# Optimization experiments

Measured on AMD Instinct MI355X. Metric: run time of the kernel, lower is better.

The kernel has to match this reference:

```python
import jax, jax.numpy as jnp
import numpy as np

B, C, H, W = 32, 512, 256, 14
NSEL = 7  # 7 even columns (0,2,..,12) on even rows, 7 odd columns (1,3,..,13) on odd rows


def setup_inputs() -> dict:
    key = jax.random.key(0)
    kx, kp = jax.random.split(key)
    x = jax.random.normal(kx, (B, C, H, W), dtype=jnp.float32)
    # per-(batch,row) random permutation of the 7 selected columns
    pkeys = jax.random.split(kp, B * H)
    perms = jax.vmap(lambda k: jax.random.permutation(k, NSEL))(pkeys)
    perms = perms.reshape(B, H, NSEL).astype(jnp.int32)
    return {"x": x, "perms": perms}


def reference(x, perms):
    # Even rows shuffle columns {0,2,...,12}; odd rows shuffle {1,3,...,13}.
    # Column of the j-th selected element on row h: 2*j + (h % 2).
    parity = (jnp.arange(H) % 2).astype(jnp.int32)[None, :, None]      # [1,H,1]
    dst = 2 * jnp.arange(NSEL, dtype=jnp.int32)[None, None, :] + parity  # [1,H,7] -> broadcast [B,H,7]
    dst = jnp.broadcast_to(dst, (B, H, NSEL))
    src = 2 * perms + parity                                            # [B,H,7]
    # Build a per-(b,h) column remap: identity, with dst <- src on shuffled slots.
    colmap = jnp.broadcast_to(jnp.arange(W, dtype=jnp.int32), (B, H, W))
    bi = jnp.arange(B, dtype=jnp.int32)[:, None, None]
    hi = jnp.arange(H, dtype=jnp.int32)[None, :, None]
    colmap = colmap.at[bi, hi, dst].set(src)                            # [B,H,W]
    # Single vectorized gather along the width axis, broadcast over channels.
    idx = jnp.broadcast_to(colmap[:, None, :, :], (B, C, H, W))
    return jnp.take_along_axis(x, idx, axis=3)
```

## Files before the change

kernel.cpp:

```cpp
#include <hip/hip_runtime.h>


#define TILE_ROWS   512
#define TILE_FLOATS (TILE_ROWS * 14)
#define TILE_V4     (TILE_FLOATS / 4)
#define WAVE_V4     448

typedef float v4f __attribute__((ext_vector_type(4)));

#define GLOAD_LDS16(gp, lp)                                                   \
    __builtin_amdgcn_global_load_lds(                                         \
        (const __attribute__((address_space(1))) void*)(gp),                  \
        (__attribute__((address_space(3))) void*)(lp), 16, 0, 0)

__global__ __launch_bounds__(256, 5) void GSRS_shuffle_pipe7_kernel(
    const float* __restrict__ x,
    const int* __restrict__ perms,
    float* __restrict__ out)
{
    __shared__ float tile[TILE_FLOATS];
    __shared__ unsigned char cmap[256][16];

    const unsigned tid  = threadIdx.x;
    const unsigned lane = tid & 63u;
    const unsigned wv   = tid >> 6;
    const unsigned tb   = blockIdx.x;
    const unsigned base = tb * TILE_FLOATS;
    const unsigned b    = tb >> 8;
    const unsigned q0   = wv * WAVE_V4 + lane;

    const unsigned r0 = wv * 128u + 2u * lane;
    const unsigned h0 = r0 & 255u;
    const int* pr = perms + b * 1792u + h0 * 7u;
    int pm[14];
#pragma unroll
    for (int j = 0; j < 7; ++j) {
        int2 t2 = *reinterpret_cast<const int2*>(pr + 2 * j);
        pm[2 * j] = t2.x; pm[2 * j + 1] = t2.y;
    }
    __builtin_amdgcn_sched_barrier(0);

    const v4f* xv = reinterpret_cast<const v4f*>(x + base);
    v4f*       tv = reinterpret_cast<v4f*>(tile);
#pragma unroll
    for (int i = 0; i < 7; ++i)
        GLOAD_LDS16(xv + q0 + i * 64, tv + q0 + i * 64);
    __builtin_amdgcn_sched_barrier(0);

    {
#pragma unroll
        for (int rr = 0; rr < 2; ++rr) {
            const unsigned h = h0 + rr;
            const unsigned p = h & 1u;
            union { unsigned char c[16]; uint4 v; } u;
#pragma unroll
            for (int w14 = 0; w14 < 14; ++w14) {
                unsigned src = (((unsigned)w14 & 1u) == p)
                    ? 2u * (unsigned)pm[rr * 7 + (w14 >> 1)] + p
                    : (unsigned)w14;
                u.c[w14] = (unsigned char)src;
            }
            u.c[14] = 0; u.c[15] = 0;
            *reinterpret_cast<uint4*>(&cmap[h][0]) = u.v;
        }
    }

    v4f vbuf[7];
#pragma unroll
    for (int i = 0; i < 7; ++i) {
        if (i < 6) {
            asm volatile("s_waitcnt vmcnt(%0)" :: "i"(5 - i) : "memory");
            __builtin_amdgcn_sched_barrier(0);
        }
        const unsigned q  = q0 + i * 64;
        unsigned lo   = q * 4u;
        unsigned lrow = lo / 14u;
        unsigned w14  = lo - lrow * 14u;
        v4f v;
#pragma unroll
        for (int k4 = 0; k4 < 4; ++k4) {
            const unsigned h   = lrow & 255u;
            const unsigned src = cmap[h][w14];
            v[k4] = tile[lrow * 14u + src];
            if (++w14 == 14u) { w14 = 0u; ++lrow; }
        }
        vbuf[i] = v;
    }

    v4f* ov = reinterpret_cast<v4f*>(out + base);
#pragma unroll
    for (int i = 0; i < 7; ++i)
        __builtin_nontemporal_store(vbuf[i], ov + q0 + i * 64);
}

extern "C" void kernel_launch(void* const* d_in, const int* in_sizes, int n_in,
                              void* d_out, int out_size, void* d_ws, size_t ws_size,
                              hipStream_t stream) {
    const float* x     = (const float*)d_in[0];
    const int*   perms = (const int*)d_in[1];
    float*       out   = (float*)d_out;

    hipLaunchKernelGGL(GSRS_shuffle_pipe7_kernel, dim3(8192), dim3(256), 0, stream,
                       x, perms, out);
}
```

Measured before the change: 72.36 us.

## Halve tile size, use per-thread row cmap and scalar coalesced stores

Shrinks each block's tile to 256 rows and doubles the grid, raising the occupancy bound to 8 blocks. Each thread builds the column map for one row, loads are issued by 56 lanes per wave in four chunks, and output is written as scalar nontemporal floats, one per lane per step. The aim is more blocks in flight and simpler index math, at the cost of narrower stores and more store instructions.

Result: no change. 72.06 us (-0.4%).

```diff
diff --git a/kernel.cpp b/kernel.cpp
--- a/kernel.cpp
+++ b/kernel.cpp
@@ -1,10 +1,10 @@
 #include <hip/hip_runtime.h>
 
 
-#define TILE_ROWS   512
+#define TILE_ROWS   256
 #define TILE_FLOATS (TILE_ROWS * 14)
-#define TILE_V4     (TILE_FLOATS / 4)
-#define WAVE_V4     448
+#define WAVE_F      896
+#define WAVE_V4     224
 
 typedef float v4f __attribute__((ext_vector_type(4)));
 
@@ -13,7 +13,7 @@
         (const __attribute__((address_space(1))) void*)(gp),                  \
         (__attribute__((address_space(3))) void*)(lp), 16, 0, 0)
 
-__global__ __launch_bounds__(256, 5) void GSRS_shuffle_pipe7_kernel(
+__global__ __launch_bounds__(256, 8) void GSRS_shuffle_win8_kernel(
     const float* __restrict__ x,
     const int* __restrict__ perms,
     float* __restrict__ out)
@@ -26,71 +26,61 @@
     const unsigned wv   = tid >> 6;
     const unsigned tb   = blockIdx.x;
     const unsigned base = tb * TILE_FLOATS;
-    const unsigned b    = tb >> 8;
-    const unsigned q0   = wv * WAVE_V4 + lane;
+    const unsigned b    = tb >> 9;
 
-    const unsigned r0 = wv * 128u + 2u * lane;
-    const unsigned h0 = r0 & 255u;
-    const int* pr = perms + b * 1792u + h0 * 7u;
-    int pm[14];
+    const int* pr = perms + b * 1792u + tid * 7u;
+    int pm[7];
 #pragma unroll
-    for (int j = 0; j < 7; ++j) {
-        int2 t2 = *reinterpret_cast<const int2*>(pr + 2 * j);
-        pm[2 * j] = t2.x; pm[2 * j + 1] = t2.y;
-    }
+    for (int j = 0; j < 7; ++j) pm[j] = pr[j];
     __builtin_amdgcn_sched_barrier(0);
 
     const v4f* xv = reinterpret_cast<const v4f*>(x + base);
     v4f*       tv = reinterpret_cast<v4f*>(tile);
+    if (lane < 56u) {
 #pragma unroll
-    for (int i = 0; i < 7; ++i)
-        GLOAD_LDS16(xv + q0 + i * 64, tv + q0 + i * 64);
+        for (int c = 0; c < 4; ++c)
+            GLOAD_LDS16(xv + wv * WAVE_V4 + c * 56 + lane,
+                        tv + wv * WAVE_V4 + c * 56 + lane);
+    }
     __builtin_amdgcn_sched_barrier(0);
 
     {
+        const unsigned p = tid & 1u;
+        union { unsigned char c[16]; uint4 v; } u;
 #pragma unroll
-        for (int rr = 0; rr < 2; ++rr) {
-            const unsigned h = h0 + rr;
-            const unsigned p = h & 1u;
-            union { unsigned char c[16]; uint4 v; } u;
-#pragma unroll
-            for (int w14 = 0; w14 < 14; ++w14) {
-                unsigned src = (((unsigned)w14 & 1u) == p)
-                    ? 2u * (unsigned)pm[rr * 7 + (w14 >> 1)] + p
-                    : (unsigned)w14;
-                u.c[w14] = (unsigned char)src;
-            }
-            u.c[14] = 0; u.c[15] = 0;
-            *reinterpret_cast<uint4*>(&cmap[h][0]) = u.v;
+        for (int w14 = 0; w14 < 14; ++w14) {
+            unsigned src = (((unsigned)w14 & 1u) == p)
+                ? 2u * (unsigned)pm[w14 >> 1] + p
+                : (unsigned)w14;
+            u.c[w14] = (unsigned char)src;
         }
+        u.c[14] = 0; u.c[15] = 0;
+        *reinterpret_cast<uint4*>(&cmap[tid][0]) = u.v;
     }
 
-    v4f vbuf[7];
+    float vbuf[14];
 #pragma unroll
-    for (int i = 0; i < 7; ++i) {
-        if (i < 6) {
-            asm volatile("s_waitcnt vmcnt(%0)" :: "i"(5 - i) : "memory");
-            __builtin_amdgcn_sched_barrier(0);
-        }
-        const unsigned q  = q0 + i * 64;
-        unsigned lo   = q * 4u;
-        unsigned lrow = lo / 14u;
-        unsigned w14  = lo - lrow * 14u;
-        v4f v;
-#pragma unroll
-        for (int k4 = 0; k4 < 4; ++k4) {
-            const unsigned h   = lrow & 255u;
-            const unsigned src = cmap[h][w14];
-            v[k4] = tile[lrow * 14u + src];
-            if (++w14 == 14u) { w14 = 0u; ++lrow; }
-        }
-        vbuf[i] = v;
+    for (int j = 0; j < 14; ++j) {
+        if (j == 0)  { asm volatile("s_waitcnt vmcnt(3)" ::: "memory");
+                       __builtin_amdgcn_sched_barrier(0); }
+        if (j == 3)  { asm volatile("s_waitcnt vmcnt(2)" ::: "memory");
+                       __builtin_amdgcn_sched_barrier(0); }
+        if (j == 7)  { asm volatile("s_waitcnt vmcnt(1)" ::: "memory");
+                       __builtin_amdgcn_sched_barrier(0); }
+        if (j == 10) { asm volatile("s_waitcnt vmcnt(0)" ::: "memory");
+                       __builtin_amdgcn_sched_barrier(0); }
+        const unsigned o    = (unsigned)j * 64u + lane;
+        const unsigned lrow = o / 14u;
+        const unsigned w14  = o - lrow * 14u;
+        const unsigned h    = wv * 64u + lrow;
+        const unsigned src  = cmap[h][w14];
+        vbuf[j] = tile[h * 14u + src];
     }
 
-    v4f* ov = reinterpret_cast<v4f*>(out + base);
+    float* op = out + base + wv * WAVE_F + lane;
 #pragma unroll
-    for (int i = 0; i < 7; ++i)
-        __builtin_nontemporal_store(vbuf[i], ov + q0 + i * 64);
+    for (int j = 0; j < 14; ++j)
+        __builtin_nontemporal_store(vbuf[j], op + j * 64);
 }
 
 extern "C" void kernel_launch(void* const* d_in, const int* in_sizes, int n_in,
@@ -100,6 +90,6 @@
     const int*   perms = (const int*)d_in[1];
     float*       out   = (float*)d_out;
 
-    hipLaunchKernelGGL(GSRS_shuffle_pipe7_kernel, dim3(8192), dim3(256), 0, stream,
+    hipLaunchKernelGGL(GSRS_shuffle_win8_kernel, dim3(16384), dim3(256), 0, stream,
                        x, perms, out);
 }
```
